# Optimization experiments

Hardware: AMD Instinct MI355X
Metric: run time of the kernel (lower is better)

The kernel has to match this reference:

```python
import jax, jax.numpy as jnp
import numpy as np

DIM = 512
H = 8
D = DIM // H  # head_dim = 64
B, N = 2, 2048


def setup_inputs() -> dict:
    key = jax.random.key(0)
    ks = jax.random.split(key, 12)
    s = 1.0 / np.sqrt(DIM)
    inp = {
        "x": jax.random.normal(ks[0], (B, N, DIM), jnp.float32),
        "geo_bias": jax.random.normal(ks[1], (B, H, N, N), jnp.float32),
        "Wq": jax.random.normal(ks[2], (DIM, DIM), jnp.float32) * s,
        "bq": jnp.zeros((DIM,), jnp.float32),
        "Wk": jax.random.normal(ks[3], (DIM, DIM), jnp.float32) * s,
        "bk": jnp.zeros((DIM,), jnp.float32),
        "Wv": jax.random.normal(ks[4], (DIM, DIM), jnp.float32) * s,
        "bv": jnp.zeros((DIM,), jnp.float32),
        "Wo": jax.random.normal(ks[5], (DIM, DIM), jnp.float32) * s,
        "bo": jnp.zeros((DIM,), jnp.float32),
    }
    return inp


def reference(x, geo_bias, Wq, bq, Wk, bk, Wv, bv, Wo, bo):
    # x: (B, N, dim); geo_bias: (B, H, N, N)
    scale = D ** -0.5
    q = (x @ Wq.T + bq).reshape(B, N, H, D)
    k = (x @ Wk.T + bk).reshape(B, N, H, D)
    v = (x @ Wv.T + bv).reshape(B, N, H, D)
    # scores: (B, H, N, N)
    attn = jnp.einsum("bihd,bjhd->bhij", q, k) * scale + geo_bias
    attn = jax.nn.softmax(attn, axis=-1)
    out = jnp.einsum("bhij,bjhd->bihd", attn, v).reshape(B, N, DIM)
    return out @ Wo.T + bo
```

## Files before the change

### kernel.cpp

```cpp
#include <hip/hip_runtime.h>
#include <math.h>

#define SCALE 0.125f

typedef __bf16 bf16;
typedef __bf16 bf16x8 __attribute__((ext_vector_type(8)));
typedef float f32x4 __attribute__((ext_vector_type(4)));

#define WS_XB   0u
#define WS_WB   4194304u
#define WS_Q    6291456u
#define WS_K    10485760u
#define WS_VT   14680064u
#define WS_AT   18874368u

__global__ __launch_bounds__(256) void convert_kernel(
    const float* __restrict__ x, const float* __restrict__ wq,
    const float* __restrict__ wk, const float* __restrict__ wv,
    const float* __restrict__ wo, bf16* __restrict__ xb, bf16* __restrict__ wb) {
  int i = blockIdx.x * 256 + threadIdx.x;
  const float4* src; bf16* dst; int off;
  if (i < 524288) { src = (const float4*)x; dst = xb; off = i; }
  else {
    int j = i - 524288;
    int wsel = j >> 16; off = j & 65535;
    const float* wl = wsel == 0 ? wq : wsel == 1 ? wk : wsel == 2 ? wv : wo;
    src = (const float4*)wl; dst = wb + (wsel << 18);
  }
  float4 v = src[off];
  union { bf16 h[4]; uint2 u; } tmp;
  tmp.h[0] = (bf16)v.x; tmp.h[1] = (bf16)v.y;
  tmp.h[2] = (bf16)v.z; tmp.h[3] = (bf16)v.w;
  ((uint2*)dst)[off] = tmp.u;
}

__global__ __launch_bounds__(256) void qkv_gemm(
    const bf16* __restrict__ xb, const bf16* __restrict__ wb,
    const float* __restrict__ bq, const float* __restrict__ bk,
    const float* __restrict__ bv, bf16* __restrict__ qws,
    bf16* __restrict__ kws, bf16* __restrict__ vtws) {
  __shared__ bf16 Al[2][128 * 40];
  __shared__ bf16 Bl[2][64 * 40];
  int t = threadIdx.x;
  int m0 = (blockIdx.x & 31) << 7;
  int n0 = (blockIdx.x >> 5) << 6;
  int lane = t & 63, w = t >> 6;
  int quad = lane >> 4, col = lane & 15;
  int mblk = (w >> 1) * 64, nblk = (w & 1) * 32;
  int arow = t >> 1, apart = (t & 1) << 1;
  int brow = t >> 2, bpart = t & 3;
  const bf16* ag = &xb[(m0 + arow) * 512 + apart * 8];
  const bf16* bg = &wb[(n0 + brow) * 512 + bpart * 8];
  f32x4 acc[4][2] = {};
  uint4 ra0 = *(const uint4*)ag;
  uint4 ra1 = *(const uint4*)(ag + 8);
  uint4 rb  = *(const uint4*)bg;
  for (int it = 0; it < 16; ++it) {
    int cur = it & 1;
    *(uint4*)&Al[cur][arow * 40 + apart * 8]     = ra0;
    *(uint4*)&Al[cur][arow * 40 + apart * 8 + 8] = ra1;
    *(uint4*)&Bl[cur][brow * 40 + bpart * 8]     = rb;
    if (it < 15) {
      int k0 = (it + 1) << 5;
      ra0 = *(const uint4*)(ag + k0);
      ra1 = *(const uint4*)(ag + k0 + 8);
      rb  = *(const uint4*)(bg + k0);
    }
    __syncthreads();
    bf16x8 af[4], bfv[2];
#pragma unroll
    for (int i = 0; i < 4; i++)
      af[i] = *(const bf16x8*)&Al[cur][(mblk + i * 16 + col) * 40 + quad * 8];
#pragma unroll
    for (int i = 0; i < 2; i++)
      bfv[i] = *(const bf16x8*)&Bl[cur][(nblk + i * 16 + col) * 40 + quad * 8];
#pragma unroll
    for (int mi = 0; mi < 4; mi++)
#pragma unroll
      for (int ni = 0; ni < 2; ni++)
        acc[mi][ni] = __builtin_amdgcn_mfma_f32_16x16x32_bf16(
            af[mi], bfv[ni], acc[mi][ni], 0, 0, 0);
  }
  for (int mi = 0; mi < 4; mi++)
    for (int ni = 0; ni < 2; ni++) {
      int n = n0 + nblk + ni * 16 + col;
      int wid = n >> 9, feat = n & 511;
      float bias = wid == 0 ? bq[feat] : wid == 1 ? bk[feat] : bv[feat];
      int h = feat >> 6, d = feat & 63;
      int mbase = m0 + mblk + mi * 16 + quad * 4;
      int bidx = mbase >> 11, seq0 = mbase & 2047;
      if (wid == 2) {
        union { bf16 h4[4]; ushort4 u4; } pk;
        for (int r = 0; r < 4; r++) pk.h4[r] = (bf16)(acc[mi][ni][r] + bias);
        *(ushort4*)&vtws[(size_t)((((bidx << 3) + h) << 6) + d) * 2048 + seq0] = pk.u4;
      } else {
        bf16* dst = wid == 0 ? qws : kws;
        for (int r = 0; r < 4; r++)
          dst[(size_t)((((bidx << 3) + h) << 11) + seq0 + r) * 64 + d] =
              (bf16)(acc[mi][ni][r] + bias);
      }
    }
}

__global__ __launch_bounds__(256, 2) void attn_kernel(
    const bf16* __restrict__ qws, const bf16* __restrict__ kws,
    const bf16* __restrict__ vtws, const float* __restrict__ gbias,
    bf16* __restrict__ attn) {
  __shared__ bf16 Kl[2][64 * 72];
  __shared__ bf16 Vl[2][64 * 72];
  __shared__ bf16 Pl[64 * 72];
  __shared__ float Bb[2][64 * 64];
  int t = threadIdx.x, lane = t & 63, w = t >> 6;
  int quad = lane >> 4, col = lane & 15;
  int bh = blockIdx.x >> 5, qt = blockIdx.x & 31;
  int q0 = qt << 6;
  const bf16* qbase = qws + (size_t)bh * 2048 * 64;
  const bf16* kbase = kws + (size_t)bh * 2048 * 64;
  const bf16* vbase = vtws + (size_t)bh * 64 * 2048;
  const float* bb = gbias + ((size_t)bh * 2048 + q0) * 2048;

  int srow = t >> 2, scol = (t & 3) << 4;
  int brow0 = t >> 4, bcol4 = t & 15;

  bf16x8 aq[2];
#pragma unroll
  for (int ks = 0; ks < 2; ++ks)
    aq[ks] = *(const bf16x8*)&qbase[(q0 + w * 16 + col) * 64 + ks * 32 + quad * 8];

  f32x4 o[4] = {};
  float mrow[4], lrow[4];
#pragma unroll
  for (int r = 0; r < 4; r++) { mrow[r] = -INFINITY; lrow[r] = 0.f; }

  *(uint4*)&Kl[0][srow * 72 + scol]     = *(const uint4*)&kbase[srow * 64 + scol];
  *(uint4*)&Kl[0][srow * 72 + scol + 8] = *(const uint4*)&kbase[srow * 64 + scol + 8];
  *(uint4*)&Vl[0][srow * 72 + scol]     = *(const uint4*)&vbase[srow * 2048 + scol];
  *(uint4*)&Vl[0][srow * 72 + scol + 8] = *(const uint4*)&vbase[srow * 2048 + scol + 8];
#pragma unroll
  for (int p = 0; p < 4; ++p) {
    int row = brow0 + (p << 4);
    int sw = (row >> 2) & 3;
    *(float4*)&Bb[0][row * 64 + ((bcol4 ^ (sw << 2)) << 2)] =
        *(const float4*)&bb[(size_t)row * 2048 + (bcol4 << 2)];
  }
  __syncthreads();

  uint4 kra, krb, vra, vrb;
  float4 br4[4];
  for (int kt = 0; kt < 32; ++kt) {
    int cur = kt & 1, nb = cur ^ 1;
    bool pre = kt < 31;
    if (pre) {
      int snxt = (kt + 1) << 6;
      kra = *(const uint4*)&kbase[(snxt + srow) * 64 + scol];
      krb = *(const uint4*)&kbase[(snxt + srow) * 64 + scol + 8];
      vra = *(const uint4*)&vbase[srow * 2048 + snxt + scol];
      vrb = *(const uint4*)&vbase[srow * 2048 + snxt + scol + 8];
#pragma unroll
      for (int p = 0; p < 4; ++p)
        br4[p] = *(const float4*)&bb[(size_t)(brow0 + (p << 4)) * 2048 + snxt + (bcol4 << 2)];
    }

    f32x4 s[4];
    __builtin_amdgcn_s_setprio(1);
#pragma unroll
    for (int nt = 0; nt < 4; ++nt) {
      f32x4 a = {};
#pragma unroll
      for (int ks = 0; ks < 2; ++ks) {
        bf16x8 bk_ = *(const bf16x8*)&Kl[cur][(nt * 16 + col) * 72 + ks * 32 + quad * 8];
        a = __builtin_amdgcn_mfma_f32_16x16x32_bf16(aq[ks], bk_, a, 0, 0, 0);
      }
      s[nt] = a;
    }
    __builtin_amdgcn_s_setprio(0);

    int rbase = (w * 16 + quad * 4) * 64;
#pragma unroll
    for (int r = 0; r < 4; r++) {
      float sv[4];
#pragma unroll
      for (int nt = 0; nt < 4; nt++)
        sv[nt] = s[nt][r] * SCALE +
                 Bb[cur][rbase + r * 64 + ((nt ^ quad) << 4) + col];
      float mx = fmaxf(fmaxf(sv[0], sv[1]), fmaxf(sv[2], sv[3]));
#pragma unroll
      for (int d = 1; d < 16; d <<= 1) mx = fmaxf(mx, __shfl_xor(mx, d));
      if (!__all(mx <= mrow[r])) {
        float mnew = fmaxf(mrow[r], mx);
        float alpha = __expf(mrow[r] - mnew);
        mrow[r] = mnew;
        lrow[r] *= alpha;
#pragma unroll
        for (int dt = 0; dt < 4; ++dt) o[dt][r] *= alpha;
      }
      float sum = 0.f;
#pragma unroll
      for (int nt = 0; nt < 4; nt++) {
        float e = __expf(sv[nt] - mrow[r]);
        s[nt][r] = e;
        sum += e;
      }
#pragma unroll
      for (int d = 1; d < 16; d <<= 1) sum += __shfl_xor(sum, d);
      lrow[r] += sum;
    }

#pragma unroll
    for (int nt = 0; nt < 4; nt++)
#pragma unroll
      for (int r = 0; r < 4; r++)
        Pl[(w * 16 + quad * 4 + r) * 72 + nt * 16 + col] = (bf16)s[nt][r];

    __builtin_amdgcn_s_setprio(1);
#pragma unroll
    for (int ks = 0; ks < 2; ++ks) {
      bf16x8 ap = *(const bf16x8*)&Pl[(w * 16 + col) * 72 + ks * 32 + quad * 8];
#pragma unroll
      for (int dt = 0; dt < 4; ++dt) {
        bf16x8 bv_ = *(const bf16x8*)&Vl[cur][(dt * 16 + col) * 72 + ks * 32 + quad * 8];
        o[dt] = __builtin_amdgcn_mfma_f32_16x16x32_bf16(ap, bv_, o[dt], 0, 0, 0);
      }
    }
    __builtin_amdgcn_s_setprio(0);

    if (pre) {
      *(uint4*)&Kl[nb][srow * 72 + scol]     = kra;
      *(uint4*)&Kl[nb][srow * 72 + scol + 8] = krb;
      *(uint4*)&Vl[nb][srow * 72 + scol]     = vra;
      *(uint4*)&Vl[nb][srow * 72 + scol + 8] = vrb;
#pragma unroll
      for (int p = 0; p < 4; ++p) {
        int row = brow0 + (p << 4);
        int sw = (row >> 2) & 3;
        *(float4*)&Bb[nb][row * 64 + ((bcol4 ^ (sw << 2)) << 2)] = br4[p];
      }
    }
    __syncthreads();
  }

  bf16* obase = attn + (size_t)(bh >> 3) * 2048 * 512 + (bh & 7) * 64;
  for (int r = 0; r < 4; r++) {
    float inv = 1.f / lrow[r];
    int gq = q0 + w * 16 + quad * 4 + r;
    for (int dt = 0; dt < 4; ++dt)
      obase[(size_t)gq * 512 + dt * 16 + col] = (bf16)(o[dt][r] * inv);
  }
}

__global__ __launch_bounds__(256) void out_gemm(
    const bf16* __restrict__ ab, const bf16* __restrict__ wob,
    const float* __restrict__ bo, float* __restrict__ out) {
  __shared__ bf16 Al[2][128 * 40];
  __shared__ bf16 Bl[2][64 * 40];
  int t = threadIdx.x;
  int m0 = (blockIdx.x & 31) << 7;
  int n0 = (blockIdx.x >> 5) << 6;
  int lane = t & 63, w = t >> 6;
  int quad = lane >> 4, col = lane & 15;
  int mblk = (w >> 1) * 64, nblk = (w & 1) * 32;
  int arow = t >> 1, apart = (t & 1) << 1;
  int brow = t >> 2, bpart = t & 3;
  const bf16* ag = &ab[(m0 + arow) * 512 + apart * 8];
  const bf16* bg = &wob[(n0 + brow) * 512 + bpart * 8];
  f32x4 acc[4][2] = {};
  uint4 ra0 = *(const uint4*)ag;
  uint4 ra1 = *(const uint4*)(ag + 8);
  uint4 rb  = *(const uint4*)bg;
  for (int it = 0; it < 16; ++it) {
    int cur = it & 1;
    *(uint4*)&Al[cur][arow * 40 + apart * 8]     = ra0;
    *(uint4*)&Al[cur][arow * 40 + apart * 8 + 8] = ra1;
    *(uint4*)&Bl[cur][brow * 40 + bpart * 8]     = rb;
    if (it < 15) {
      int k0 = (it + 1) << 5;
      ra0 = *(const uint4*)(ag + k0);
      ra1 = *(const uint4*)(ag + k0 + 8);
      rb  = *(const uint4*)(bg + k0);
    }
    __syncthreads();
    bf16x8 af[4], bfv[2];
#pragma unroll
    for (int i = 0; i < 4; i++)
      af[i] = *(const bf16x8*)&Al[cur][(mblk + i * 16 + col) * 40 + quad * 8];
#pragma unroll
    for (int i = 0; i < 2; i++)
      bfv[i] = *(const bf16x8*)&Bl[cur][(nblk + i * 16 + col) * 40 + quad * 8];
#pragma unroll
    for (int mi = 0; mi < 4; mi++)
#pragma unroll
      for (int ni = 0; ni < 2; ni++)
        acc[mi][ni] = __builtin_amdgcn_mfma_f32_16x16x32_bf16(
            af[mi], bfv[ni], acc[mi][ni], 0, 0, 0);
  }
  for (int mi = 0; mi < 4; mi++)
    for (int ni = 0; ni < 2; ni++)
      for (int r = 0; r < 4; r++) {
        int m = m0 + mblk + mi * 16 + quad * 4 + r;
        int n = n0 + nblk + ni * 16 + col;
        out[(size_t)m * 512 + n] = acc[mi][ni][r] + bo[n];
      }
}

extern "C" void kernel_launch(void* const* d_in, const int* in_sizes, int n_in,
                              void* d_out, int out_size, void* d_ws, size_t ws_size,
                              hipStream_t stream) {
  const float* x  = (const float*)d_in[0];
  const float* gb = (const float*)d_in[1];
  const float* Wq = (const float*)d_in[2];
  const float* bq = (const float*)d_in[3];
  const float* Wk = (const float*)d_in[4];
  const float* bk = (const float*)d_in[5];
  const float* Wv = (const float*)d_in[6];
  const float* bv = (const float*)d_in[7];
  const float* Wo = (const float*)d_in[8];
  const float* bo = (const float*)d_in[9];
  float* out = (float*)d_out;
  char* ws = (char*)d_ws;
  bf16* xb   = (bf16*)(ws + WS_XB);
  bf16* wb   = (bf16*)(ws + WS_WB);
  bf16* qws  = (bf16*)(ws + WS_Q);
  bf16* kws  = (bf16*)(ws + WS_K);
  bf16* vtws = (bf16*)(ws + WS_VT);
  bf16* at   = (bf16*)(ws + WS_AT);

  hipLaunchKernelGGL(convert_kernel, dim3(3072), dim3(256), 0, stream,
                     x, Wq, Wk, Wv, Wo, xb, wb);
  hipLaunchKernelGGL(qkv_gemm, dim3(768), dim3(256), 0, stream,
                     xb, wb, bq, bk, bv, qws, kws, vtws);
  hipLaunchKernelGGL(attn_kernel, dim3(512), dim3(256), 0, stream,
                     qws, kws, vtws, gb, at);
  hipLaunchKernelGGL(out_gemm, dim3(256), dim3(256), 0, stream,
                     at, wb + 3 * 262144, bo, out);
}
```

Baseline: 429.6 us.

## Stage attention K/V/bias tiles via direct global-to-LDS loads with XOR swizzle

Replaces the register-staged double-buffer prefetch of K, V and geo_bias tiles with global_load_lds direct-to-LDS transfers, using unpadded tiles with an XOR swizzle to avoid bank conflicts. This removes the VGPR staging and the separate LDS store phase, which should lower register pressure and instruction count. It also defers the cross-lane row-sum reduction to the epilogue instead of doing it every tile. The risk is that the async LDS writes are only ordered by the per-iteration __syncthreads, and the swizzle mapping must stay consistent between writers and readers.

```diff
diff --git a/kernel.cpp b/kernel.cpp
--- a/kernel.cpp
+++ b/kernel.cpp
@@ -6,6 +6,13 @@
 typedef __bf16 bf16;
 typedef __bf16 bf16x8 __attribute__((ext_vector_type(8)));
 typedef float f32x4 __attribute__((ext_vector_type(4)));
+typedef unsigned int u32;
+
+__device__ __forceinline__ void gl_lds16(const void* g, void* l) {
+  __builtin_amdgcn_global_load_lds(
+      (const __attribute__((address_space(1))) u32*)g,
+      (__attribute__((address_space(3))) u32*)l, 16, 0, 0);
+}
 
 #define WS_XB   0u
 #define WS_WB   4194304u
@@ -106,10 +113,10 @@
     const bf16* __restrict__ qws, const bf16* __restrict__ kws,
     const bf16* __restrict__ vtws, const float* __restrict__ gbias,
     bf16* __restrict__ attn) {
-  __shared__ bf16 Kl[2][64 * 72];
-  __shared__ bf16 Vl[2][64 * 72];
+  __shared__ bf16 Kl[2][64 * 64];
+  __shared__ bf16 Vl[2][64 * 64];
+  __shared__ float Bb[2][64 * 64];
   __shared__ bf16 Pl[64 * 72];
-  __shared__ float Bb[2][64 * 64];
   int t = threadIdx.x, lane = t & 63, w = t >> 6;
   int quad = lane >> 4, col = lane & 15;
   int bh = blockIdx.x >> 5, qt = blockIdx.x & 31;
@@ -119,8 +126,8 @@
   const bf16* vbase = vtws + (size_t)bh * 64 * 2048;
   const float* bb = gbias + ((size_t)bh * 2048 + q0) * 2048;
 
-  int srow = t >> 2, scol = (t & 3) << 4;
-  int brow0 = t >> 4, bcol4 = t & 15;
+  int lr = lane >> 3, lc = lane & 7, swc = lc ^ lr;
+  int brow = lane >> 4, bw0 = (lane & 15) << 2;
 
   bf16x8 aq[2];
 #pragma unroll
@@ -128,61 +135,62 @@
     aq[ks] = *(const bf16x8*)&qbase[(q0 + w * 16 + col) * 64 + ks * 32 + quad * 8];
 
   f32x4 o[4] = {};
+  f32x4 s[4];
   float mrow[4], lrow[4];
 #pragma unroll
   for (int r = 0; r < 4; r++) { mrow[r] = -INFINITY; lrow[r] = 0.f; }
 
-  *(uint4*)&Kl[0][srow * 72 + scol]     = *(const uint4*)&kbase[srow * 64 + scol];
-  *(uint4*)&Kl[0][srow * 72 + scol + 8] = *(const uint4*)&kbase[srow * 64 + scol + 8];
-  *(uint4*)&Vl[0][srow * 72 + scol]     = *(const uint4*)&vbase[srow * 2048 + scol];
-  *(uint4*)&Vl[0][srow * 72 + scol + 8] = *(const uint4*)&vbase[srow * 2048 + scol + 8];
-#pragma unroll
-  for (int p = 0; p < 4; ++p) {
-    int row = brow0 + (p << 4);
-    int sw = (row >> 2) & 3;
-    *(float4*)&Bb[0][row * 64 + ((bcol4 ^ (sw << 2)) << 2)] =
-        *(const float4*)&bb[(size_t)row * 2048 + (bcol4 << 2)];
-  }
+#pragma unroll
+  for (int c = 0; c < 2; ++c) {
+    gl_lds16(&kbase[(size_t)(w * 16 + c * 8 + lr) * 64 + swc * 8],
+             &Kl[0][(w * 16 + c * 8) * 64]);
+    gl_lds16(&vbase[(size_t)(w * 16 + c * 8 + lr) * 2048 + swc * 8],
+             &Vl[0][(w * 16 + c * 8) * 64]);
+  }
+#pragma unroll
+  for (int c = 0; c < 4; ++c)
+    gl_lds16(&bb[(size_t)(w * 16 + c * 4 + brow) * 2048 + (bw0 ^ (c << 4))],
+             &Bb[0][(w * 16 + c * 4) * 64]);
   __syncthreads();
 
-  uint4 kra, krb, vra, vrb;
-  float4 br4[4];
   for (int kt = 0; kt < 32; ++kt) {
     int cur = kt & 1, nb = cur ^ 1;
-    bool pre = kt < 31;
-    if (pre) {
-      int snxt = (kt + 1) << 6;
-      kra = *(const uint4*)&kbase[(snxt + srow) * 64 + scol];
-      krb = *(const uint4*)&kbase[(snxt + srow) * 64 + scol + 8];
-      vra = *(const uint4*)&vbase[srow * 2048 + snxt + scol];
-      vrb = *(const uint4*)&vbase[srow * 2048 + snxt + scol + 8];
-#pragma unroll
-      for (int p = 0; p < 4; ++p)
-        br4[p] = *(const float4*)&bb[(size_t)(brow0 + (p << 4)) * 2048 + snxt + (bcol4 << 2)];
-    }
-
-    f32x4 s[4];
+    if (kt < 31) {
+      int s0 = (kt + 1) << 6;
+#pragma unroll
+      for (int c = 0; c < 2; ++c) {
+        gl_lds16(&kbase[(size_t)(s0 + w * 16 + c * 8 + lr) * 64 + swc * 8],
+                 &Kl[nb][(w * 16 + c * 8) * 64]);
+        gl_lds16(&vbase[(size_t)(w * 16 + c * 8 + lr) * 2048 + s0 + swc * 8],
+                 &Vl[nb][(w * 16 + c * 8) * 64]);
+      }
+#pragma unroll
+      for (int c = 0; c < 4; ++c)
+        gl_lds16(&bb[(size_t)(w * 16 + c * 4 + brow) * 2048 + s0 + (bw0 ^ (c << 4))],
+                 &Bb[nb][(w * 16 + c * 4) * 64]);
+    }
+
     __builtin_amdgcn_s_setprio(1);
 #pragma unroll
     for (int nt = 0; nt < 4; ++nt) {
       f32x4 a = {};
 #pragma unroll
       for (int ks = 0; ks < 2; ++ks) {
-        bf16x8 bk_ = *(const bf16x8*)&Kl[cur][(nt * 16 + col) * 72 + ks * 32 + quad * 8];
+        bf16x8 bk_ = *(const bf16x8*)&Kl[cur][(nt * 16 + col) * 64 +
+                                              (((ks * 4 + quad) ^ (col & 7)) << 3)];
         a = __builtin_amdgcn_mfma_f32_16x16x32_bf16(aq[ks], bk_, a, 0, 0, 0);
       }
       s[nt] = a;
     }
     __builtin_amdgcn_s_setprio(0);
 
-    int rbase = (w * 16 + quad * 4) * 64;
+    int rb = (w * 16 + quad * 4) * 64;
 #pragma unroll
     for (int r = 0; r < 4; r++) {
       float sv[4];
 #pragma unroll
       for (int nt = 0; nt < 4; nt++)
-        sv[nt] = s[nt][r] * SCALE +
-                 Bb[cur][rbase + r * 64 + ((nt ^ quad) << 4) + col];
+        sv[nt] = s[nt][r] * SCALE + Bb[cur][rb + r * 64 + (((nt ^ quad) << 4) | col)];
       float mx = fmaxf(fmaxf(sv[0], sv[1]), fmaxf(sv[2], sv[3]));
 #pragma unroll
       for (int d = 1; d < 16; d <<= 1) mx = fmaxf(mx, __shfl_xor(mx, d));
@@ -194,16 +202,14 @@
 #pragma unroll
         for (int dt = 0; dt < 4; ++dt) o[dt][r] *= alpha;
       }
-      float sum = 0.f;
+      float ls = 0.f;
 #pragma unroll
       for (int nt = 0; nt < 4; nt++) {
         float e = __expf(sv[nt] - mrow[r]);
         s[nt][r] = e;
-        sum += e;
-      }
-#pragma unroll
-      for (int d = 1; d < 16; d <<= 1) sum += __shfl_xor(sum, d);
-      lrow[r] += sum;
+        ls += e;
+      }
+      lrow[r] += ls;
     }
 
 #pragma unroll
@@ -218,31 +224,23 @@
       bf16x8 ap = *(const bf16x8*)&Pl[(w * 16 + col) * 72 + ks * 32 + quad * 8];
 #pragma unroll
       for (int dt = 0; dt < 4; ++dt) {
-        bf16x8 bv_ = *(const bf16x8*)&Vl[cur][(dt * 16 + col) * 72 + ks * 32 + quad * 8];
+        bf16x8 bv_ = *(const bf16x8*)&Vl[cur][(dt * 16 + col) * 64 +
+                                              (((ks * 4 + quad) ^ (col & 7)) << 3)];
         o[dt] = __builtin_amdgcn_mfma_f32_16x16x32_bf16(ap, bv_, o[dt], 0, 0, 0);
       }
     }
     __builtin_amdgcn_s_setprio(0);
-
-    if (pre) {
-      *(uint4*)&Kl[nb][srow * 72 + scol]     = kra;
-      *(uint4*)&Kl[nb][srow * 72 + scol + 8] = krb;
-      *(uint4*)&Vl[nb][srow * 72 + scol]     = vra;
-      *(uint4*)&Vl[nb][srow * 72 + scol + 8] = vrb;
-#pragma unroll
-      for (int p = 0; p < 4; ++p) {
-        int row = brow0 + (p << 4);
-        int sw = (row >> 2) & 3;
-        *(float4*)&Bb[nb][row * 64 + ((bcol4 ^ (sw << 2)) << 2)] = br4[p];
-      }
-    }
     __syncthreads();
   }
 
   bf16* obase = attn + (size_t)(bh >> 3) * 2048 * 512 + (bh & 7) * 64;
+#pragma unroll
   for (int r = 0; r < 4; r++) {
+#pragma unroll
+    for (int d = 1; d < 16; d <<= 1) lrow[r] += __shfl_xor(lrow[r], d);
     float inv = 1.f / lrow[r];
     int gq = q0 + w * 16 + quad * 4 + r;
+#pragma unroll
     for (int dt = 0; dt < 4; ++dt)
       obase[(size_t)gq * 512 + dt * 16 + col] = (bf16)(o[dt][r] * inv);
   }
```

Result: no change. 429.2 us (-0.1%).
